# Kernel optimization log

Hardware: AMD Instinct MI355X
Metric: run time of the kernel (lower is better)

Reference implementation:

```python
import jax, jax.numpy as jnp
import numpy as np

B, M, D = 8, 1024, 768          # batch, tokens, model dim
N, P = 32, 32                   # experts, slots per expert (N*P == M)
K = 8                           # mix_k (router top-k)
H = 2048                        # expert MLP hidden dim
EPS = 1e-12


def setup_inputs() -> dict:
    key = jax.random.key(0)
    ks = jax.random.split(key, 6)
    std_d = 1.0 / np.sqrt(D)
    std_h = 1.0 / np.sqrt(H)
    return {
        "x": jax.random.normal(ks[0], (B, M, D), jnp.float32),
        "cluster_assignments": jax.random.randint(ks[1], (B, M, K), 0, N),
        "phi": jax.random.normal(ks[2], (D, N, P), jnp.float32) * std_d,
        "scale": jnp.ones((1,), jnp.float32),
        "w1": jax.random.normal(ks[3], (N, D, H), jnp.float32) * std_d,
        "b1": jnp.zeros((N, H), jnp.float32),
        "w2": jax.random.normal(ks[4], (N, H, D), jnp.float32) * std_h,
        "b2": jnp.zeros((N, D), jnp.float32),
    }


def _seg_mean(vals, idx, num_segments):
    # index_reduce(..., 'mean', include_self=False): empty segments stay 0
    s = jax.ops.segment_sum(vals, idx, num_segments=num_segments)
    c = jax.ops.segment_sum(jnp.ones((vals.shape[0], 1), vals.dtype), idx,
                            num_segments=num_segments)
    return jnp.where(c > 0, s / jnp.maximum(c, 1.0), 0.0)


def _compute_acmoe(x_flat, top_assign):
    # MAD-based per-cluster, per-dim scaling (mad=True, mix_weights=False)
    mean_kd = _seg_mean(x_flat, top_assign, N)                 # [N, D]
    centered = jnp.abs(x_flat - mean_kd[top_assign])           # [B*M, D]
    w_mad = _seg_mean(centered, top_assign, N)                 # [N, D]
    W = 1.0 / (w_mad + 0.35)
    top_clamp = 5.0 * W.mean()
    W = jnp.minimum(W, top_clamp)
    W = W / W.mean()
    return W[top_assign]                                       # [B*M, D]


def reference(x, cluster_assignments, phi, scale, w1, b1, w2, b2):
    # normalize tokens (dim=2) and phi (dim=0), scale phi
    xn = x / jnp.maximum(jnp.linalg.norm(x, axis=-1, keepdims=True), EPS)
    phin = scale * phi / jnp.maximum(jnp.linalg.norm(phi, axis=0, keepdims=True), EPS)

    # ACMoE feature re-weighting (no-grad in original)
    top_assign = cluster_assignments.reshape(-1, K)[:, 0]       # [B*M]
    Mw = jax.lax.stop_gradient(_compute_acmoe(
        jax.lax.stop_gradient(xn.reshape(-1, D)), top_assign))
    xn = (xn.reshape(-1, D) * Mw).reshape(B, M, D)

    logits = jnp.einsum('bmd,dnp->bmnp', xn, phin)              # [B,M,N,P]
    aff = logits.reshape(B, M, N * P)
    mixing_weights, slot_assignments = jax.lax.top_k(aff, K)    # [B,M,K]
    new_clusters = slot_assignments // P

    disp = jax.nn.softmax(logits, axis=1)                       # over tokens m
    comb = jax.nn.softmax(aff, axis=-1).reshape(B, M, N, P)     # over (n,p)

    xs = jnp.einsum('bmd,bmnp->bnpd', xn, disp)                 # [B,N,P,D]
    # per-expert MLP, batched over expert axis n
    h = jnp.einsum('bnpd,ndh->bnph', xs, w1) + b1[None, :, None, :]
    h = jax.nn.gelu(h, approximate=False)
    ys = jnp.einsum('bnph,nhd->bnpd', h, w2) + b2[None, :, None, :]

    y = jnp.einsum('bnpd,bmnp->bmd', ys, comb)                  # [B,M,D]
    return y, mixing_weights, new_clusters
```

## Files before the change

kernel.cpp:

```cpp
#include <hip/hip_runtime.h>
#include <cmath>

#define NB    8
#define MTOK  1024
#define BMT   8192
#define DD    768
#define NEXP  32
#define PSLOT 32
#define NP    1024
#define KTOP  8
#define HH    2048

#define SLICES 128
#define TPS    64

typedef unsigned short ushort;
typedef __attribute__((ext_vector_type(8))) short short8v;
typedef __attribute__((ext_vector_type(4))) short short4v;
typedef __attribute__((ext_vector_type(4))) float f32x4;

__device__ __forceinline__ ushort bf16_rne(float x) {
    unsigned u = __float_as_uint(x);
    unsigned r = (u + 0x7FFFu + ((u >> 16) & 1u)) >> 16;
    return (ushort)r;
}
__device__ __forceinline__ float bf16_to_f(ushort h) {
    return __uint_as_float(((unsigned)h) << 16);
}
__device__ __forceinline__ void split2(float x, ushort& hi, ushort& lo) {
    hi = bf16_rne(x);
    lo = bf16_rne(x - bf16_to_f(hi));
}
__device__ __forceinline__ unsigned cvt_pk_bf16(float a, float b) {
    unsigned r;
    asm volatile("v_cvt_pk_bf16_f32 %0, %1, %2" : "=v"(r) : "v"(a), "v"(b));
    return r;
}

__device__ __forceinline__ void gl_lds16(const ushort* g, ushort* l) {
    __builtin_amdgcn_global_load_lds(
        (const __attribute__((address_space(1))) void*)g,
        (__attribute__((address_space(3))) void*)l, 16, 0, 0);
}

__global__ __launch_bounds__(256) void norm_x(const float* __restrict__ x, float* __restrict__ xn) {
    int tok = blockIdx.x;
    int t = threadIdx.x;
    const float* p = x + (long)tok * DD;
    float v0 = p[t], v1 = p[t + 256], v2 = p[t + 512];
    float ss = v0 * v0 + v1 * v1 + v2 * v2;
#pragma unroll
    for (int o = 32; o; o >>= 1) ss += __shfl_xor(ss, o);
    __shared__ float sred[4];
    if ((t & 63) == 0) sred[t >> 6] = ss;
    __syncthreads();
    ss = sred[0] + sred[1] + sred[2] + sred[3];
    float inv = 1.0f / fmaxf(sqrtf(ss), 1e-12f);
    float* q = xn + (long)tok * DD;
    q[t] = v0 * inv; q[t + 256] = v1 * inv; q[t + 512] = v2 * inv;
}

__global__ __launch_bounds__(256) void norm_phi_T(const float* __restrict__ phi, const float* __restrict__ scale,
                                                  ushort* __restrict__ phT_hi, ushort* __restrict__ phT_lo) {
    int np = blockIdx.x;
    int t = threadIdx.x;
    float ss = 0.f;
    for (int d = t; d < DD; d += 256) {
        float v = phi[(long)d * NP + np];
        ss += v * v;
    }
#pragma unroll
    for (int o = 32; o; o >>= 1) ss += __shfl_xor(ss, o);
    __shared__ float sred[4];
    if ((t & 63) == 0) sred[t >> 6] = ss;
    __syncthreads();
    ss = sred[0] + sred[1] + sred[2] + sred[3];
    float sc = scale[0] / fmaxf(sqrtf(ss), 1e-12f);
    for (int d = t; d < DD; d += 256) {
        float v = phi[(long)d * NP + np] * sc;
        ushort h, l; split2(v, h, l);
        phT_hi[(long)np * DD + d] = h;
        phT_lo[(long)np * DD + d] = l;
    }
}

__global__ __launch_bounds__(256) void cluster_sum(const float* __restrict__ xn, const int* __restrict__ ca,
                                                   float* __restrict__ spart, float* __restrict__ cntpart) {
    __shared__ float s[NEXP][256];
    __shared__ float cnt[NEXP];
    int chunk = blockIdx.x, slice = blockIdx.y, t = threadIdx.x;
#pragma unroll
    for (int n = 0; n < NEXP; ++n) s[n][t] = 0.f;
    if (t < NEXP) cnt[t] = 0.f;
    __syncthreads();
    int tok0 = slice * TPS;
    for (int i = 0; i < TPS; ++i) {
        int tok = tok0 + i;
        int a = ca[tok * KTOP];
        float v = xn[(long)tok * DD + chunk * 256 + t];
        s[a][t] += v;
        if (chunk == 0 && t == 0) cnt[a] += 1.f;
    }
    __syncthreads();
    for (int n = 0; n < NEXP; ++n)
        spart[(long)slice * (NEXP * DD) + n * DD + chunk * 256 + t] = s[n][t];
    if (chunk == 0 && t < NEXP) cntpart[slice * NEXP + t] = cnt[t];
}

__global__ __launch_bounds__(256) void reduce_parts(const float* __restrict__ part, float* __restrict__ outv,
                                                    const float* __restrict__ cntpart, float* __restrict__ ccnt,
                                                    int doCnt) {
    int i = blockIdx.x * 256 + threadIdx.x;
    float s = 0.f;
#pragma unroll 8
    for (int sl = 0; sl < SLICES; ++sl) s += part[(long)sl * (NEXP * DD) + i];
    outv[i] = s;
    if (doCnt && i < NEXP) {
        float c = 0.f;
#pragma unroll 8
        for (int sl = 0; sl < SLICES; ++sl) c += cntpart[sl * NEXP + i];
        ccnt[i] = c;
    }
}

__global__ __launch_bounds__(256) void cluster_mad(const float* __restrict__ xn, const int* __restrict__ ca,
                                                   const float* __restrict__ csum, const float* __restrict__ ccnt,
                                                   float* __restrict__ mpart) {
    __shared__ float md[NEXP][256];
    __shared__ float mean[NEXP][256];
    int chunk = blockIdx.x, slice = blockIdx.y, t = threadIdx.x;
#pragma unroll
    for (int n = 0; n < NEXP; ++n) {
        float c = ccnt[n];
        mean[n][t] = (c > 0.f) ? csum[n * DD + chunk * 256 + t] / c : 0.f;
        md[n][t] = 0.f;
    }
    __syncthreads();
    int tok0 = slice * TPS;
    for (int i = 0; i < TPS; ++i) {
        int tok = tok0 + i;
        int a = ca[tok * KTOP];
        float v = xn[(long)tok * DD + chunk * 256 + t];
        md[a][t] += fabsf(v - mean[a][t]);
    }
    __syncthreads();
    for (int n = 0; n < NEXP; ++n)
        mpart[(long)slice * (NEXP * DD) + n * DD + chunk * 256 + t] = md[n][t];
}

__global__ __launch_bounds__(1024) void compute_W(const float* __restrict__ cmad, const float* __restrict__ ccnt,
                                                  float* __restrict__ W) {
    __shared__ float s[16];
    int t = threadIdx.x;
    auto block_sum = [&](float v) -> float {
#pragma unroll
        for (int o = 32; o; o >>= 1) v += __shfl_xor(v, o);
        if ((t & 63) == 0) s[t >> 6] = v;
        __syncthreads();
        float tot = 0.f;
#pragma unroll
        for (int i = 0; i < 16; ++i) tot += s[i];
        __syncthreads();
        return tot;
    };
    const int TOT = NEXP * DD;
    float p = 0.f;
    for (int i = t; i < TOT; i += 1024) {
        int n = i / DD;
        float c = ccnt[n];
        float wm = (c > 0.f) ? cmad[i] / c : 0.f;
        p += 1.f / (wm + 0.35f);
    }
    float mean1 = block_sum(p) / (float)TOT;
    float clamp = 5.f * mean1;
    p = 0.f;
    for (int i = t; i < TOT; i += 1024) {
        int n = i / DD;
        float c = ccnt[n];
        float wm = (c > 0.f) ? cmad[i] / c : 0.f;
        p += fminf(1.f / (wm + 0.35f), clamp);
    }
    float mean2 = block_sum(p) / (float)TOT;
    float inv2 = 1.f / mean2;
    for (int i = t; i < TOT; i += 1024) {
        int n = i / DD;
        float c = ccnt[n];
        float wm = (c > 0.f) ? cmad[i] / c : 0.f;
        W[i] = fminf(1.f / (wm + 0.35f), clamp) * inv2;
    }
}

__global__ __launch_bounds__(192) void apply_W(float* __restrict__ xn, const int* __restrict__ ca,
                                               const float* __restrict__ W,
                                               ushort* __restrict__ hi, ushort* __restrict__ lo) {
    int tok = blockIdx.x;
    long d4 = (long)tok * DD + threadIdx.x * 4;
    int a = ca[tok * KTOP];
    float4 v = *reinterpret_cast<float4*>(xn + d4);
    float4 w = *reinterpret_cast<const float4*>(W + a * DD + threadIdx.x * 4);
    v.x *= w.x; v.y *= w.y; v.z *= w.z; v.w *= w.w;
    *reinterpret_cast<float4*>(xn + d4) = v;
    ushort h0,h1,h2,h3,l0,l1,l2,l3;
    split2(v.x,h0,l0); split2(v.y,h1,l1); split2(v.z,h2,l2); split2(v.w,h3,l3);
    *reinterpret_cast<short4v*>(hi + d4) = short4v{(short)h0,(short)h1,(short)h2,(short)h3};
    *reinterpret_cast<short4v*>(lo + d4) = short4v{(short)l0,(short)l1,(short)l2,(short)l3};
}

template <bool F32>
__global__ __launch_bounds__(256) void make_T(const void* __restrict__ srcv, ushort* __restrict__ dst,
                                              int R, int C) {
    __shared__ ushort tile[64][65];
    int z = blockIdx.z;
    int c0 = blockIdx.x * 64, r0 = blockIdx.y * 64;
    int tr = threadIdx.x >> 4;
    int tc4 = (threadIdx.x & 15) * 4;
    long base = (long)z * R * C;
#pragma unroll
    for (int i = 0; i < 4; ++i) {
        int r = tr + i * 16;
        if constexpr (F32) {
            const float* s = (const float*)srcv;
            float4 v = *reinterpret_cast<const float4*>(s + base + (long)(r0 + r) * C + c0 + tc4);
            tile[r][tc4 + 0] = bf16_rne(v.x); tile[r][tc4 + 1] = bf16_rne(v.y);
            tile[r][tc4 + 2] = bf16_rne(v.z); tile[r][tc4 + 3] = bf16_rne(v.w);
        } else {
            const ushort* s = (const ushort*)srcv;
            short4v v = *reinterpret_cast<const short4v*>(s + base + (long)(r0 + r) * C + c0 + tc4);
            tile[r][tc4 + 0] = (ushort)v.x; tile[r][tc4 + 1] = (ushort)v.y;
            tile[r][tc4 + 2] = (ushort)v.z; tile[r][tc4 + 3] = (ushort)v.w;
        }
    }
    __syncthreads();
#pragma unroll
    for (int i = 0; i < 4; ++i) {
        int oc = tr + i * 16;
        short4v o = short4v{(short)tile[tc4 + 0][oc], (short)tile[tc4 + 1][oc],
                            (short)tile[tc4 + 2][oc], (short)tile[tc4 + 3][oc]};
        *reinterpret_cast<short4v*>(dst + base + (long)(c0 + oc) * R + r0 + tc4) = o;
    }
}

template <int MODE, int AMAP, int EPI, bool CBF16, int CMAP>
__global__ __launch_bounds__((MODE == 1) ? 256 : 512) void gemm2(
    const ushort* __restrict__ Ah_g, const ushort* __restrict__ Al_g,
    const float*  __restrict__ Bf_g,
    const ushort* __restrict__ Bh_g, const ushort* __restrict__ Bl_g,
    float* __restrict__ Cf, ushort* __restrict__ Cb,
    int K, int lda, int ldb, int ldc,
    long sA, long sB, long sC,
    const float* __restrict__ bias, int biasStride) {
    constexpr bool PAIR = (MODE == 1);
    constexpr int THR  = PAIR ? 256 : 512;
    constexpr int BUFS = 12288;
    constexpr int BOFF = PAIR ? 4096 : 8192;
    constexpr int BM   = PAIR ? 64 : 256;
    constexpr int MI   = PAIR ? 2 : 4;
    __shared__ __attribute__((aligned(16))) ushort lds[3 * BUFS];

    int orig = blockIdx.x + gridDim.x * (blockIdx.y + gridDim.y * blockIdx.z);
    int nwg = gridDim.x * gridDim.y * gridDim.z;
    int wg = (orig & 7) * (nwg >> 3) + (orig >> 3);
    int bx = wg % gridDim.x;
    int rest = wg / gridDim.x;
    int by = rest % gridDim.y;
    int z  = rest / gridDim.y;
    const int m0 = by * BM;
    const int n0 = bx * 128;

    const int tid = threadIdx.x, lane = tid & 63, w = tid >> 6;
    const int wr = w >> 1, wc = w & 1;
    const int lr = lane & 15, kh = lane >> 4;

    const int NCA = PAIR ? 1 : 2;
    long arowA[2]; int kOffA[2];
#pragma unroll
    for (int i = 0; i < NCA; ++i) {
        int c = i * THR + tid;
        int r = c >> 2, sp = c & 3;
        kOffA[i] = (sp ^ ((r >> 1) & 3)) << 3;
        int rg = m0 + r;
        if constexpr (AMAP == 0) arowA[i] = (long)z * sA + (long)rg * lda;
        else arowA[i] = ((long)(rg >> 5) * 1024 + (long)z * 32 + (rg & 31)) * (long)lda;
    }
    long browB[2]; int kOffB[2];
#pragma unroll
    for (int i = 0; i < 2; ++i) {
        int c = i * 256 + tid;
        if (c < 512) {
            int r = c >> 2, sp = c & 3;
            kOffB[i] = (sp ^ ((r >> 1) & 3)) << 3;
            browB[i] = (long)z * sB + (long)(n0 + r) * ldb;
        }
    }
    const int kqh = tid & 15, nq = tid >> 4;

    f32x4 acc[MI][4];
#pragma unroll
    for (int i = 0; i < MI; ++i)
#pragma unroll
        for (int j = 0; j < 4; ++j) acc[i][j] = (f32x4)(0.f);

    auto stageA = [&](int buf, int kk0) {
        const int bb = buf * BUFS;
        if constexpr (MODE == 1) {
            gl_lds16(Ah_g + arowA[0] + kk0 + kOffA[0], &lds[bb + (w * 64) * 8]);
            gl_lds16(Al_g + arowA[0] + kk0 + kOffA[0], &lds[bb + 2048 + (w * 64) * 8]);
#pragma unroll
            for (int i = 0; i < 2; ++i) {
                int base = bb + 4096 + (i * 256 + w * 64) * 8;
                gl_lds16(Bh_g + browB[i] + kk0 + kOffB[i], &lds[base]);
                gl_lds16(Bl_g + browB[i] + kk0 + kOffB[i], &lds[base + 4096]);
            }
        } else if constexpr (MODE == 0) {
#pragma unroll
            for (int i = 0; i < 2; ++i)
                gl_lds16(Ah_g + arowA[i] + kk0 + kOffA[i], &lds[bb + (i * THR + w * 64) * 8]);
            gl_lds16(Bh_g + browB[0] + kk0 + kOffB[0], &lds[bb + BOFF + (w * 64) * 8]);
        } else {
#pragma unroll
            for (int i = 0; i < 2; ++i)
                gl_lds16(Ah_g + arowA[i] + kk0 + kOffA[i], &lds[bb + (i * THR + w * 64) * 8]);
        }
    };

    auto loadB = [&](float4 (&rB)[2], int kk0) {
#pragma unroll
        for (int dk = 0; dk < 2; ++dk)
            rB[dk] = *reinterpret_cast<const float4*>(
                Bf_g + (long)z * sB + (long)(kk0 + kqh * 2 + dk) * ldb + n0 + nq * 4);
    };

    auto bwrite = [&](int buf, float4 (&rB)[2]) {
        unsigned p[4];
        p[0] = cvt_pk_bf16(rB[0].x, rB[1].x);
        p[1] = cvt_pk_bf16(rB[0].y, rB[1].y);
        p[2] = cvt_pk_bf16(rB[0].z, rB[1].z);
        p[3] = cvt_pk_bf16(rB[0].w, rB[1].w);
        int k = kqh * 2;
        int s = k >> 3, kin = k & 7;
#pragma unroll
        for (int dn = 0; dn < 4; ++dn) {
            int n = nq * 4 + dn;
            int phys = s ^ ((n >> 1) & 3);
            int off = buf * BUFS + BOFF + n * 32 + phys * 8 + kin;
            *reinterpret_cast<unsigned*>(&lds[off]) = p[dn];
        }
    };

    auto compute = [&](int buf) {
        const int aB = buf * BUFS;
        const int bB = buf * BUFS + BOFF;
        short8v bh[4], bl[4];
#pragma unroll
        for (int nj = 0; nj < 4; ++nj) {
            int rb = wc * 64 + nj * 16 + lr;
            int off = bB + rb * 32 + ((kh ^ ((rb >> 1) & 3)) << 3);
            bh[nj] = *reinterpret_cast<const short8v*>(&lds[off]);
            if constexpr (PAIR) bl[nj] = *reinterpret_cast<const short8v*>(&lds[off + 4096]);
        }
#pragma unroll
        for (int mi = 0; mi < MI; ++mi) {
            int ra = wr * (PAIR ? 32 : 64) + mi * 16 + lr;
            int off = aB + ra * 32 + ((kh ^ ((ra >> 1) & 3)) << 3);
            short8v ah = *reinterpret_cast<const short8v*>(&lds[off]);
            if constexpr (PAIR) {
                short8v al = *reinterpret_cast<const short8v*>(&lds[off + 2048]);
#pragma unroll
                for (int nj = 0; nj < 4; ++nj) {
                    acc[mi][nj] = __builtin_amdgcn_mfma_f32_16x16x32_bf16(ah, bh[nj], acc[mi][nj], 0, 0, 0);
                    acc[mi][nj] = __builtin_amdgcn_mfma_f32_16x16x32_bf16(ah, bl[nj], acc[mi][nj], 0, 0, 0);
                    acc[mi][nj] = __builtin_amdgcn_mfma_f32_16x16x32_bf16(al, bh[nj], acc[mi][nj], 0, 0, 0);
                }
            } else {
#pragma unroll
                for (int nj = 0; nj < 4; ++nj)
                    acc[mi][nj] = __builtin_amdgcn_mfma_f32_16x16x32_bf16(ah, bh[nj], acc[mi][nj], 0, 0, 0);
            }
        }
    };

    const int nt = K >> 5;
    if constexpr (MODE == 0 || MODE == 1) {
        stageA(0, 0);
        stageA(1, 32);
        if constexpr (MODE == 1) { asm volatile("s_waitcnt vmcnt(6)" ::: "memory"); }
        else                     { asm volatile("s_waitcnt vmcnt(3)" ::: "memory"); }
        __builtin_amdgcn_s_barrier();
        __builtin_amdgcn_sched_barrier(0);
        int cc = 0, cn2 = 2;
        for (int t = 0; t < nt; ++t) {
            bool deep = (t + 2 < nt);
            if (deep) stageA(cn2, (t + 2) << 5);
            compute(cc);
            if (deep) {
                if constexpr (MODE == 1) { asm volatile("s_waitcnt vmcnt(6)" ::: "memory"); }
                else                     { asm volatile("s_waitcnt vmcnt(3)" ::: "memory"); }
            } else {
                asm volatile("s_waitcnt vmcnt(0)" ::: "memory");
            }
            if (t + 1 < nt) {
                __builtin_amdgcn_s_barrier();
                __builtin_amdgcn_sched_barrier(0);
            }
            cc = (cc == 2) ? 0 : cc + 1;
            cn2 = (cn2 == 2) ? 0 : cn2 + 1;
        }
    } else {
        float4 rBa[2], rBb[2];
        loadB(rBa, 0);
        bwrite(0, rBa);
        stageA(0, 0);
        stageA(1, 32);
        loadB(rBb, 32);
        asm volatile("s_waitcnt vmcnt(4) lgkmcnt(0)" ::: "memory");
        __builtin_amdgcn_s_barrier();
        __builtin_amdgcn_sched_barrier(0);
        int cc = 0, cn1 = 1, cn2 = 2;
        auto iter = [&](int t, float4 (&ld)[2], float4 (&wr_)[2]) {
            bool deep = (t + 2 < nt);
            if (deep) { stageA(cn2, (t + 2) << 5); loadB(ld, (t + 2) << 5); }
            compute(cc);
            if (t + 1 < nt) bwrite(cn1, wr_);
            if (deep) { asm volatile("s_waitcnt vmcnt(4) lgkmcnt(0)" ::: "memory"); }
            else      { asm volatile("s_waitcnt vmcnt(0) lgkmcnt(0)" ::: "memory"); }
            if (t + 1 < nt) {
                __builtin_amdgcn_s_barrier();
                __builtin_amdgcn_sched_barrier(0);
            }
            cc = (cc == 2) ? 0 : cc + 1;
            cn1 = (cn1 == 2) ? 0 : cn1 + 1;
            cn2 = (cn2 == 2) ? 0 : cn2 + 1;
        };
        for (int t = 0; t < nt; t += 2) {
            iter(t, rBa, rBb);
            iter(t + 1, rBb, rBa);
        }
    }

#pragma unroll
    for (int mi = 0; mi < MI; ++mi)
#pragma unroll
        for (int j = 0; j < 4; ++j) {
            int rg = m0 + wr * (PAIR ? 32 : 64) + mi * 16 + kh * 4 + j;
            long roff;
            if constexpr (CMAP == 1) roff = ((long)(rg >> 5) * 1024 + (long)z * 32 + (rg & 31)) * (long)ldc;
            else                     roff = (long)z * sC + (long)rg * ldc;
#pragma unroll
            for (int nj = 0; nj < 4; ++nj) {
                int col = n0 + wc * 64 + nj * 16 + lr;
                float v = acc[mi][nj][j];
                if constexpr (EPI >= 1) v += bias[(long)z * biasStride + col];
                if constexpr (EPI == 2) v = 0.5f * v * (1.0f + erff(v * 0.70710678118654752f));
                if constexpr (CBF16) Cb[roff + col] = bf16_rne(v);
                else                 Cf[roff + col] = v;
            }
        }
}

__global__ __launch_bounds__(64) void row_topk(const float* __restrict__ logits,
                                               float* __restrict__ mix_out, float* __restrict__ clus_out,
                                               ushort* __restrict__ comb) {
    int row = blockIdx.x;
    int lane = threadIdx.x;
    const float* p = logits + (long)row * NP;
    float v[16];
#pragma unroll
    for (int i = 0; i < 16; ++i) v[i] = p[lane + i * 64];
    float mx = v[0];
#pragma unroll
    for (int i = 1; i < 16; ++i) mx = fmaxf(mx, v[i]);
#pragma unroll
    for (int o = 32; o; o >>= 1) mx = fmaxf(mx, __shfl_xor(mx, o));
    float s = 0.f;
#pragma unroll
    for (int i = 0; i < 16; ++i) s += __expf(v[i] - mx);
#pragma unroll
    for (int o = 32; o; o >>= 1) s += __shfl_xor(s, o);
    float inv = 1.0f / s;
    ushort* crow = comb + (long)row * NP;
#pragma unroll
    for (int i = 0; i < 16; ++i)
        crow[lane + i * 64] = bf16_rne(__expf(v[i] - mx) * inv);
#pragma unroll
    for (int k = 0; k < KTOP; ++k) {
        float bv = -INFINITY; int bi = 1 << 30;
#pragma unroll
        for (int i = 0; i < 16; ++i) {
            if (v[i] > bv) { bv = v[i]; bi = lane + i * 64; }
        }
#pragma unroll
        for (int o = 32; o; o >>= 1) {
            float ov = __shfl_xor(bv, o); int oi = __shfl_xor(bi, o);
            if (ov > bv || (ov == bv && oi < bi)) { bv = ov; bi = oi; }
        }
        int owner = bi & 63, slot = bi >> 6;
        if (lane == owner) {
#pragma unroll
            for (int i = 0; i < 16; ++i) if (slot == i) v[i] = -INFINITY;
        }
        if (lane == k) {
            mix_out[(long)row * KTOP + k] = bv;
            clus_out[(long)row * KTOP + k] = (float)(bi >> 5);
        }
    }
}

__global__ __launch_bounds__(256) void col_stats_part(const float* __restrict__ logits,
                                                      float* __restrict__ pmax, float* __restrict__ psum) {
    int b = blockIdx.z, ms = blockIdx.y, npc = blockIdx.x;
    int np = npc * 256 + threadIdx.x;
    const float* p = logits + ((long)b * MTOK + ms * 128) * NP + np;
    float mx = -INFINITY, s = 0.f;
    for (int m = 0; m < 128; ++m) {
        float v = p[(long)m * NP];
        float nm = fmaxf(mx, v);
        s = s * __expf(mx - nm) + __expf(v - nm);
        mx = nm;
    }
    long o = ((long)b * 8 + ms) * NP + np;
    pmax[o] = mx; psum[o] = s;
}

__global__ __launch_bounds__(256) void make_dispT(const float* __restrict__ logits,
                                                  const float* __restrict__ pmax, const float* __restrict__ psum,
                                                  ushort* __restrict__ dispT) {
    __shared__ float tile[64][65];
    __shared__ float smax[64], sinv[64];
    int b = blockIdx.z, np0 = blockIdx.x * 64, m0 = blockIdx.y * 64;
    int tr = threadIdx.x >> 6, tc = threadIdx.x & 63;
    if (threadIdx.x < 64) {
        int np = np0 + threadIdx.x;
        float mx = -INFINITY;
#pragma unroll
        for (int ms = 0; ms < 8; ++ms) mx = fmaxf(mx, pmax[((long)b * 8 + ms) * NP + np]);
        float s = 0.f;
#pragma unroll
        for (int ms = 0; ms < 8; ++ms) {
            long o = ((long)b * 8 + ms) * NP + np;
            s += psum[o] * __expf(pmax[o] - mx);
        }
        smax[threadIdx.x] = mx;
        sinv[threadIdx.x] = 1.0f / s;
    }
    const float* src = logits + ((long)b * MTOK + m0) * NP + np0;
#pragma unroll
    for (int i = 0; i < 16; ++i) {
        int m = tr * 16 + i;
        tile[m][tc] = src[(long)m * NP + tc];
    }
    __syncthreads();
#pragma unroll
    for (int i = 0; i < 16; ++i) {
        int npl = tr * 16 + i;
        float v = __expf(tile[tc][npl] - smax[npl]) * sinv[npl];
        dispT[((long)b * NP + np0 + npl) * MTOK + (m0 + tc)] = bf16_rne(v);
    }
}

extern "C" void kernel_launch(void* const* d_in, const int* in_sizes, int n_in,
                              void* d_out, int out_size, void* d_ws, size_t ws_size,
                              hipStream_t stream) {
    const float* x    = (const float*)d_in[0];
    const int*   ca   = (const int*)d_in[1];
    const float* phi  = (const float*)d_in[2];
    const float* scale= (const float*)d_in[3];
    const float* w1   = (const float*)d_in[4];
    const float* b1   = (const float*)d_in[5];
    const float* w2   = (const float*)d_in[6];
    const float* b2   = (const float*)d_in[7];
    float* out = (float*)d_out;
    float* ws  = (float*)d_ws;

    float*  xn       = ws;
    float*  logits   = xn + 6291456;
    ushort* xnp_hi   = (ushort*)(logits + 8388608);
    ushort* xnp_lo   = xnp_hi + 6291456;
    ushort* phT_hi   = xnp_lo + 6291456;
    ushort* phT_lo   = phT_hi + 786432;
    ushort* dispT_bf = phT_lo + 786432;
    ushort* comb_bf  = dispT_bf + 8388608;
    ushort* xs_bf    = comb_bf + 8388608;
    ushort* h_bf     = xs_bf + 6291456;
    ushort* xnT_bf   = h_bf + 16777216;
    ushort* ysT_bf   = xnT_bf + 6291456;
    float*  stats    = (float*)(ysT_bf + 6291456);
    float* pmax      = stats;
    float* psum      = pmax + 65536;
    float* csum      = psum + 65536;
    float* cmad      = csum + 24576;
    float* Wbuf      = cmad + 24576;
    float* ccnt      = Wbuf + 24576;
    float* cntpart   = ccnt + 64;
    float* spart     = cntpart + 4096;
    float* mpart     = spart + 3145728;
    float* ys        = xn;

    float* out_y    = out;
    float* out_mix  = out + 6291456;
    float* out_clus = out + 6291456 + 65536;

    norm_x<<<BMT, 256, 0, stream>>>(x, xn);
    norm_phi_T<<<NP, 256, 0, stream>>>(phi, scale, phT_hi, phT_lo);

    cluster_sum<<<dim3(3, SLICES), 256, 0, stream>>>(xn, ca, spart, cntpart);
    reduce_parts<<<96, 256, 0, stream>>>(spart, csum, cntpart, ccnt, 1);
    cluster_mad<<<dim3(3, SLICES), 256, 0, stream>>>(xn, ca, csum, ccnt, mpart);
    reduce_parts<<<96, 256, 0, stream>>>(mpart, cmad, nullptr, nullptr, 0);
    compute_W<<<1, 1024, 0, stream>>>(cmad, ccnt, Wbuf);
    apply_W<<<BMT, 192, 0, stream>>>(xn, ca, Wbuf, xnp_hi, xnp_lo);

    make_T<false><<<dim3(12, 16, NB), 256, 0, stream>>>(xnp_hi, xnT_bf, MTOK, DD);

    gemm2<1, 0, 0, false, 0><<<dim3(8, 128, 1), 256, 0, stream>>>(
        xnp_hi, xnp_lo, nullptr, phT_hi, phT_lo, logits, nullptr,
        DD, DD, DD, NP, 0, 0, 0, nullptr, 0);

    row_topk<<<BMT, 64, 0, stream>>>(logits, out_mix, out_clus, comb_bf);
    col_stats_part<<<dim3(4, 8, NB), 256, 0, stream>>>(logits, pmax, psum);
    make_dispT<<<dim3(16, 16, NB), 256, 0, stream>>>(logits, pmax, psum, dispT_bf);

    gemm2<0, 0, 0, true, 0><<<dim3(6, 4, NB), 512, 0, stream>>>(
        dispT_bf, nullptr, nullptr, xnT_bf, nullptr, nullptr, xs_bf,
        MTOK, MTOK, MTOK, DD,
        (long)NP * MTOK, (long)DD * MTOK, (long)NP * DD, nullptr, 0);

    gemm2<2, 1, 2, true, 0><<<dim3(16, 1, NEXP), 512, 0, stream>>>(
        xs_bf, nullptr, w1, nullptr, nullptr, nullptr, h_bf,
        DD, DD, HH, HH,
        0, (long)DD * HH, (long)256 * HH, b1, HH);

    gemm2<2, 0, 1, false, 1><<<dim3(6, 1, NEXP), 512, 0, stream>>>(
        h_bf, nullptr, w2, nullptr, nullptr, ys, nullptr,
        HH, HH, DD, DD,
        (long)256 * HH, (long)HH * DD, 0, b2, DD);

    make_T<true><<<dim3(12, 16, NB), 256, 0, stream>>>(ys, ysT_bf, MTOK, DD);

    gemm2<0, 0, 0, false, 0><<<dim3(6, 4, NB), 512, 0, stream>>>(
        comb_bf, nullptr, nullptr, ysT_bf, nullptr, out_y, nullptr,
        NP, NP, NP, DD,
        (long)MTOK * NP, (long)DD * NP, (long)MTOK * DD, nullptr, 0);
}
```

Before: 466.1 us.

## Fuse column softmax statistics into logits GEMM epilogue and drop xn writeback

Computes per-column max and sum-of-exp partials for the token-axis softmax inside the logits GEMM epilogue, using an LDS reduction across warps. This removes the separate col_stats_part kernel that reread the full logits tensor. apply_W also stops writing the reweighted xn back to global memory, since only the bf16 hi/lo splits are consumed later. make_dispT now merges 16 partials per column instead of 8, and the GEMM epilogue gains extra syncs and exp work.

```diff
diff --git a/kernel.cpp b/kernel.cpp
--- a/kernel.cpp
+++ b/kernel.cpp
@@ -190,16 +190,15 @@
     }
 }
 
-__global__ __launch_bounds__(192) void apply_W(float* __restrict__ xn, const int* __restrict__ ca,
+__global__ __launch_bounds__(192) void apply_W(const float* __restrict__ xn, const int* __restrict__ ca,
                                                const float* __restrict__ W,
                                                ushort* __restrict__ hi, ushort* __restrict__ lo) {
     int tok = blockIdx.x;
     long d4 = (long)tok * DD + threadIdx.x * 4;
     int a = ca[tok * KTOP];
-    float4 v = *reinterpret_cast<float4*>(xn + d4);
+    float4 v = *reinterpret_cast<const float4*>(xn + d4);
     float4 w = *reinterpret_cast<const float4*>(W + a * DD + threadIdx.x * 4);
     v.x *= w.x; v.y *= w.y; v.z *= w.z; v.w *= w.w;
-    *reinterpret_cast<float4*>(xn + d4) = v;
     ushort h0,h1,h2,h3,l0,l1,l2,l3;
     split2(v.x,h0,l0); split2(v.y,h1,l1); split2(v.z,h2,l2); split2(v.w,h3,l3);
     *reinterpret_cast<short4v*>(hi + d4) = short4v{(short)h0,(short)h1,(short)h2,(short)h3};
@@ -240,7 +239,7 @@
     }
 }
 
-template <int MODE, int AMAP, int EPI, bool CBF16, int CMAP>
+template <int MODE, int AMAP, int EPI, bool CBF16, int CMAP, bool CSTAT>
 __global__ __launch_bounds__((MODE == 1) ? 256 : 512) void gemm2(
     const ushort* __restrict__ Ah_g, const ushort* __restrict__ Al_g,
     const float*  __restrict__ Bf_g,
@@ -248,7 +247,8 @@
     float* __restrict__ Cf, ushort* __restrict__ Cb,
     int K, int lda, int ldb, int ldc,
     long sA, long sB, long sC,
-    const float* __restrict__ bias, int biasStride) {
+    const float* __restrict__ bias, int biasStride,
+    float* __restrict__ pmaxO, float* __restrict__ psumO) {
     constexpr bool PAIR = (MODE == 1);
     constexpr int THR  = PAIR ? 256 : 512;
     constexpr int BUFS = 12288;
@@ -455,6 +455,61 @@
                 else                 Cf[roff + col] = v;
             }
         }
+
+    if constexpr (CSTAT) {
+        float* red = (float*)lds;
+        __syncthreads();
+        float tmax[4];
+#pragma unroll
+        for (int nj = 0; nj < 4; ++nj) {
+            float m = acc[0][nj][0];
+#pragma unroll
+            for (int mi = 0; mi < MI; ++mi)
+#pragma unroll
+                for (int j = 0; j < 4; ++j) m = fmaxf(m, acc[mi][nj][j]);
+            m = fmaxf(m, __shfl_xor(m, 16));
+            m = fmaxf(m, __shfl_xor(m, 32));
+            tmax[nj] = m;
+        }
+        if (kh == 0) {
+#pragma unroll
+            for (int nj = 0; nj < 4; ++nj)
+                red[((wr * 2 + wc) * 16 + lr) * 4 + nj] = tmax[nj];
+        }
+        __syncthreads();
+        float tsum[4];
+#pragma unroll
+        for (int nj = 0; nj < 4; ++nj) {
+            float m = fmaxf(red[((0 * 2 + wc) * 16 + lr) * 4 + nj],
+                            red[((1 * 2 + wc) * 16 + lr) * 4 + nj]);
+            tmax[nj] = m;
+            float s = 0.f;
+#pragma unroll
+            for (int mi = 0; mi < MI; ++mi)
+#pragma unroll
+                for (int j = 0; j < 4; ++j) s += __expf(acc[mi][nj][j] - m);
+            s += __shfl_xor(s, 16);
+            s += __shfl_xor(s, 32);
+            tsum[nj] = s;
+        }
+        __syncthreads();
+        if (kh == 0) {
+#pragma unroll
+            for (int nj = 0; nj < 4; ++nj)
+                red[((wr * 2 + wc) * 16 + lr) * 4 + nj] = tsum[nj];
+        }
+        __syncthreads();
+        if (w < 2 && kh == 0) {
+#pragma unroll
+            for (int nj = 0; nj < 4; ++nj) {
+                int col = n0 + wc * 64 + nj * 16 + lr;
+                float stot = red[((0 * 2 + wc) * 16 + lr) * 4 + nj] +
+                             red[((1 * 2 + wc) * 16 + lr) * 4 + nj];
+                pmaxO[(long)by * NP + col] = tmax[nj];
+                psumO[(long)by * NP + col] = stot;
+            }
+        }
+    }
 }
 
 __global__ __launch_bounds__(64) void row_topk(const float* __restrict__ logits,
@@ -503,22 +558,6 @@
             clus_out[(long)row * KTOP + k] = (float)(bi >> 5);
         }
     }
-}
-
-__global__ __launch_bounds__(256) void col_stats_part(const float* __restrict__ logits,
-                                                      float* __restrict__ pmax, float* __restrict__ psum) {
-    int b = blockIdx.z, ms = blockIdx.y, npc = blockIdx.x;
-    int np = npc * 256 + threadIdx.x;
-    const float* p = logits + ((long)b * MTOK + ms * 128) * NP + np;
-    float mx = -INFINITY, s = 0.f;
-    for (int m = 0; m < 128; ++m) {
-        float v = p[(long)m * NP];
-        float nm = fmaxf(mx, v);
-        s = s * __expf(mx - nm) + __expf(v - nm);
-        mx = nm;
-    }
-    long o = ((long)b * 8 + ms) * NP + np;
-    pmax[o] = mx; psum[o] = s;
 }
 
 __global__ __launch_bounds__(256) void make_dispT(const float* __restrict__ logits,
@@ -532,11 +571,11 @@
         int np = np0 + threadIdx.x;
         float mx = -INFINITY;
 #pragma unroll
-        for (int ms = 0; ms < 8; ++ms) mx = fmaxf(mx, pmax[((long)b * 8 + ms) * NP + np]);
+        for (int ms = 0; ms < 16; ++ms) mx = fmaxf(mx, pmax[((long)(b * 16 + ms)) * NP + np]);
         float s = 0.f;
 #pragma unroll
-        for (int ms = 0; ms < 8; ++ms) {
-            long o = ((long)b * 8 + ms) * NP + np;
+        for (int ms = 0; ms < 16; ++ms) {
+            long o = ((long)(b * 16 + ms)) * NP + np;
             s += psum[o] * __expf(pmax[o] - mx);
         }
         smax[threadIdx.x] = mx;
@@ -585,8 +624,8 @@
     ushort* ysT_bf   = xnT_bf + 6291456;
     float*  stats    = (float*)(ysT_bf + 6291456);
     float* pmax      = stats;
-    float* psum      = pmax + 65536;
-    float* csum      = psum + 65536;
+    float* psum      = pmax + 131072;
+    float* csum      = psum + 131072;
     float* cmad      = csum + 24576;
     float* Wbuf      = cmad + 24576;
     float* ccnt      = Wbuf + 24576;
@@ -611,33 +650,32 @@
 
     make_T<false><<<dim3(12, 16, NB), 256, 0, stream>>>(xnp_hi, xnT_bf, MTOK, DD);
 
-    gemm2<1, 0, 0, false, 0><<<dim3(8, 128, 1), 256, 0, stream>>>(
+    gemm2<1, 0, 0, false, 0, true><<<dim3(8, 128, 1), 256, 0, stream>>>(
         xnp_hi, xnp_lo, nullptr, phT_hi, phT_lo, logits, nullptr,
-        DD, DD, DD, NP, 0, 0, 0, nullptr, 0);
+        DD, DD, DD, NP, 0, 0, 0, nullptr, 0, pmax, psum);
 
     row_topk<<<BMT, 64, 0, stream>>>(logits, out_mix, out_clus, comb_bf);
-    col_stats_part<<<dim3(4, 8, NB), 256, 0, stream>>>(logits, pmax, psum);
     make_dispT<<<dim3(16, 16, NB), 256, 0, stream>>>(logits, pmax, psum, dispT_bf);
 
-    gemm2<0, 0, 0, true, 0><<<dim3(6, 4, NB), 512, 0, stream>>>(
+    gemm2<0, 0, 0, true, 0, false><<<dim3(6, 4, NB), 512, 0, stream>>>(
         dispT_bf, nullptr, nullptr, xnT_bf, nullptr, nullptr, xs_bf,
         MTOK, MTOK, MTOK, DD,
-        (long)NP * MTOK, (long)DD * MTOK, (long)NP * DD, nullptr, 0);
-
-    gemm2<2, 1, 2, true, 0><<<dim3(16, 1, NEXP), 512, 0, stream>>>(
+        (long)NP * MTOK, (long)DD * MTOK, (long)NP * DD, nullptr, 0, nullptr, nullptr);
+
+    gemm2<2, 1, 2, true, 0, false><<<dim3(16, 1, NEXP), 512, 0, stream>>>(
         xs_bf, nullptr, w1, nullptr, nullptr, nullptr, h_bf,
         DD, DD, HH, HH,
-        0, (long)DD * HH, (long)256 * HH, b1, HH);
-
-    gemm2<2, 0, 1, false, 1><<<dim3(6, 1, NEXP), 512, 0, stream>>>(
+        0, (long)DD * HH, (long)256 * HH, b1, HH, nullptr, nullptr);
+
+    gemm2<2, 0, 1, false, 1, false><<<dim3(6, 1, NEXP), 512, 0, stream>>>(
         h_bf, nullptr, w2, nullptr, nullptr, ys, nullptr,
         HH, HH, DD, DD,
-        (long)256 * HH, (long)HH * DD, 0, b2, DD);
+        (long)256 * HH, (long)HH * DD, 0, b2, DD, nullptr, nullptr);
 
     make_T<true><<<dim3(12, 16, NB), 256, 0, stream>>>(ys, ysT_bf, MTOK, DD);
 
-    gemm2<0, 0, 0, false, 0><<<dim3(6, 4, NB), 512, 0, stream>>>(
+    gemm2<0, 0, 0, false, 0, false><<<dim3(6, 4, NB), 512, 0, stream>>>(
         comb_bf, nullptr, nullptr, ysT_bf, nullptr, out_y, nullptr,
         NP, NP, NP, DD,
-        (long)MTOK * NP, (long)DD * NP, (long)MTOK * DD, nullptr, 0);
-}
+        (long)MTOK * NP, (long)DD * NP, (long)MTOK * DD, nullptr, 0, nullptr, nullptr);
+}
```

After: 456.7 us, median of 2. -2.0%, faster.
